# Kernel tuning notes

Measured on AMD Instinct MI355X. Metric: run time of the kernel, lower is better.

Reference implementation:

```python
import jax, jax.numpy as jnp
import numpy as np

DEPTH, DIM, DH, QH, KH = 8, 512, 64, 16, 8
B, T, S = 2, 16, 257
NUM_SPECIAL, TBE, CLAMP = 1, 4, 50.0
DI = int(DIM * 4 * 2 / 3)  # 1365
EPS = 1.1920929e-07  # torch.finfo(float32).eps used by torch RMSNorm


def _rms(x, w):
    return x * jax.lax.rsqrt(jnp.mean(jnp.square(x), -1, keepdims=True) + EPS) * w


def _l2norm(x):
    return x / jnp.maximum(jnp.linalg.norm(x, axis=-1, keepdims=True), 1e-12)


def _rotary(n):
    inv = 1.0 / (10000.0 ** (jnp.arange(0, DH, 2, dtype=jnp.float32) / DH))
    f = jnp.arange(n, dtype=jnp.float32)[:, None] * inv[None, :]
    return jnp.concatenate([f, f], -1)  # [n, DH]


def _apply_rot(rot, x):
    x1, x2 = jnp.split(x, 2, -1)
    half = jnp.concatenate([-x2, x1], -1)
    return x * jnp.cos(rot) + half * jnp.sin(rot)


def _attend(q, k, v, mask=None, causal=False):
    # q: [b, QH, n, d]; k, v: [b, KH, n, d]; GQA with groups = QH//KH
    b, hq, n, d = q.shape
    h = k.shape[1]
    g = hq // h
    qg = q.reshape(b, h, g, n, d)
    sim = jnp.einsum('bhgid,bhjd->bhgij', qg, k) * (d ** -0.5)
    sim = jnp.tanh(sim / CLAMP) * CLAMP  # softclamp
    neg = -jnp.finfo(sim.dtype).max
    if mask is not None:
        sim = jnp.where(mask, sim, neg)
    if causal:
        j = sim.shape[-1]
        cm = jnp.triu(jnp.ones((n, j), bool), j - n + 1)
        sim = jnp.where(cm, neg, sim)
    attn = jax.nn.softmax(sim, axis=-1)
    out = jnp.einsum('bhgij,bhjd->bhgid', attn, v)
    return out.reshape(b, hq, n, d)


def _attn_block(x, nw, wq, wk, wv, qg, kg, wo, rot, mask, causal):
    bn, n, _ = x.shape
    h = _rms(x, nw)
    q = (h @ wq).reshape(bn, n, QH, DH).transpose(0, 2, 1, 3)
    k = (h @ wk).reshape(bn, n, KH, DH).transpose(0, 2, 1, 3)
    v = (h @ wv).reshape(bn, n, KH, DH).transpose(0, 2, 1, 3)
    sc = DH ** 0.5
    q = _l2norm(q) * ((qg + 1.0) * sc)[:, None, :]
    k = _l2norm(k) * ((kg + 1.0) * sc)[:, None, :]
    if rot is not None:
        q = _apply_rot(rot, q)
        k = _apply_rot(rot, k)
    o = _attend(q, k, v, mask=mask, causal=causal)
    o = o.transpose(0, 2, 1, 3).reshape(bn, n, QH * DH)
    return o @ wo


def _ff(x, nw, win, bin_, wout, bout):
    h = _rms(x, nw)
    a, g = jnp.split(h @ win + bin_, 2, -1)
    return (a * jax.nn.gelu(g, approximate=False)) @ wout + bout


def setup_inputs() -> dict:
    key = jax.random.key(0)
    ks = jax.random.split(key, 8)
    s = 0.02
    return {
        'tokens': jax.random.normal(ks[0], (B, T, S, DIM), jnp.float32),
        'attn_norm_w': jnp.ones((DEPTH, DIM), jnp.float32),
        'Wq': jax.random.normal(ks[1], (DEPTH, DIM, QH * DH), jnp.float32) * s,
        'Wk': jax.random.normal(ks[2], (DEPTH, DIM, KH * DH), jnp.float32) * s,
        'Wv': jax.random.normal(ks[3], (DEPTH, DIM, KH * DH), jnp.float32) * s,
        'q_gamma': jnp.zeros((DEPTH, QH, DH), jnp.float32),
        'k_gamma': jnp.zeros((DEPTH, KH, DH), jnp.float32),
        'Wo': jax.random.normal(ks[4], (DEPTH, QH * DH, DIM), jnp.float32) * s,
        'ff_norm_w': jnp.ones((DEPTH, DIM), jnp.float32),
        'W_in': jax.random.normal(ks[5], (DEPTH, DIM, 2 * DI), jnp.float32) * s,
        'b_in': jnp.zeros((DEPTH, 2 * DI), jnp.float32),
        'W_out': jax.random.normal(ks[6], (DEPTH, DI, DIM), jnp.float32) * s,
        'b_out': jnp.zeros((DEPTH, DIM), jnp.float32),
        'final_w': jnp.ones((DIM,), jnp.float32),
    }


def reference(tokens, attn_norm_w, Wq, Wk, Wv, q_gamma, k_gamma, Wo,
              ff_norm_w, W_in, b_in, W_out, b_out, final_w):
    x = tokens  # [B, T, S, D]
    # spatial special-token mask: normal tokens cannot attend to special (rightmost) tokens
    idx = jnp.arange(S)
    is_sp = idx >= (S - NUM_SPECIAL)
    sp_mask = ~((~is_sp[:, None]) & is_sp[None, :])  # [S, S]
    sp_mask = sp_mask[None, None, None]  # broadcast over (b, h, g)
    rot = _rotary(T)
    for l in range(DEPTH):
        is_time = (l + 1) % TBE == 0
        if is_time:
            y = x.transpose(0, 2, 1, 3).reshape(B * S, T, DIM)
            o = _attn_block(y, attn_norm_w[l], Wq[l], Wk[l], Wv[l], q_gamma[l],
                            k_gamma[l], Wo[l], rot=rot, mask=None, causal=True)
            x = x + o.reshape(B, S, T, DIM).transpose(0, 2, 1, 3)
        else:
            y = x.reshape(B * T, S, DIM)
            o = _attn_block(y, attn_norm_w[l], Wq[l], Wk[l], Wv[l], q_gamma[l],
                            k_gamma[l], Wo[l], rot=None, mask=sp_mask, causal=False)
            x = x + o.reshape(B, T, S, DIM)
        x = x + _ff(x, ff_norm_w[l], W_in[l], b_in[l], W_out[l], b_out[l])
    return _rms(x, final_w)
```

## Files before the change

### kernel.cpp

```cpp
#include <hip/hip_runtime.h>
#include <hip/hip_bf16.h>
#include <math.h>

typedef __attribute__((ext_vector_type(8))) short short8;
typedef __attribute__((ext_vector_type(4))) float f32x4;
typedef __hip_bfloat16 bf16;

#define BB 2
#define TT 16
#define SSQ 257
#define DIMD 512
#define NROWS 8224
#define DII 1365
#define DI2 2730
#define FNPAD 2816
#define GLULD 1408
#define SKP 288
#define EPSR 1.1920929e-07f

__device__ __forceinline__ void async16(const void* g, const void* l) {
    __builtin_amdgcn_global_load_lds(
        (const __attribute__((address_space(1))) void*)g,
        (__attribute__((address_space(3))) void*)l, 16, 0, 0);
}

__device__ __forceinline__ short f2bfs(float x) {
    bf16 h = __float2bfloat16(x);
    return *reinterpret_cast<short*>(&h);
}

__global__ void wtrans_layer(const float* __restrict__ wq, const float* __restrict__ wk,
                             const float* __restrict__ wv, const float* __restrict__ wo,
                             const float* __restrict__ win, const float* __restrict__ wout,
                             bf16* __restrict__ dqkv, bf16* __restrict__ dwo,
                             bf16* __restrict__ dwin, bf16* __restrict__ dwout) {
    __shared__ float tile[32][33];
    int bid = blockIdx.x;
    const float* src; bf16* dst; int K, M, Kpad, interleave = 0, local;
    if (bid < 512)       { src = wq;   dst = dqkv;            K = 512;  M = 1024; Kpad = 512;  local = bid; }
    else if (bid < 768)  { src = wk;   dst = dqkv + 1024*512; K = 512;  M = 512;  Kpad = 512;  local = bid - 512; }
    else if (bid < 1024) { src = wv;   dst = dqkv + 1536*512; K = 512;  M = 512;  Kpad = 512;  local = bid - 768; }
    else if (bid < 1536) { src = wo;   dst = dwo;             K = 1024; M = 512;  Kpad = 1024; local = bid - 1024; }
    else if (bid < 2944) { src = win;  dst = dwin;            K = 512;  M = 2730; Kpad = 512;  local = bid - 1536; interleave = 1; }
    else                 { src = wout; dst = dwout;           K = 1365; M = 512;  Kpad = 1408; local = bid - 2944; }
    int tilesx = Kpad >> 5;
    int k0 = (local % tilesx) * 32, m0 = (local / tilesx) * 32;
    int tx = threadIdx.x & 31, ty = threadIdx.x >> 5;
    #pragma unroll
    for (int i = 0; i < 4; ++i) {
        int k = k0 + ty + 8 * i, m = m0 + tx;
        tile[ty + 8 * i][tx] = (k < K && m < M) ? src[(size_t)k * M + m] : 0.f;
    }
    __syncthreads();
    #pragma unroll
    for (int i = 0; i < 4; ++i) {
        int n = m0 + ty + 8 * i, k = k0 + tx;
        int nd = n;
        if (interleave) nd = (n < DII) ? 2 * n : ((n < DI2) ? 2 * (n - DII) + 1 : n);
        dst[(size_t)nd * Kpad + k] = __float2bfloat16(tile[tx][ty + 8 * i]);
    }
}

template<int BF16OUT>
__global__ __launch_bounds__(256)
void rms_kernel(const float* __restrict__ x, const float* __restrict__ w,
                void* __restrict__ out, int perm) {
    int wave = threadIdx.x >> 6, lane = threadIdx.x & 63;
    int r = blockIdx.x * 4 + wave;
    int src = r;
    if (perm) {
        int t = r & 15; int rs = r >> 4; int s = rs % SSQ; int b = rs / SSQ;
        src = (b * TT + t) * SSQ + s;
    }
    const float4* xr = (const float4*)(x + (size_t)src * DIMD) + lane * 2;
    float4 a = xr[0], c = xr[1];
    float ss = a.x*a.x + a.y*a.y + a.z*a.z + a.w*a.w
             + c.x*c.x + c.y*c.y + c.z*c.z + c.w*c.w;
    ss += __shfl_xor(ss, 1);  ss += __shfl_xor(ss, 2);  ss += __shfl_xor(ss, 4);
    ss += __shfl_xor(ss, 8);  ss += __shfl_xor(ss, 16); ss += __shfl_xor(ss, 32);
    float sc = rsqrtf(ss * (1.f / DIMD) + EPSR);
    const float4* wr = (const float4*)w + lane * 2;
    float4 wa = wr[0], wb = wr[1];
    if (BF16OUT) {
        short8 v;
        v[0] = f2bfs(a.x * sc * wa.x); v[1] = f2bfs(a.y * sc * wa.y);
        v[2] = f2bfs(a.z * sc * wa.z); v[3] = f2bfs(a.w * sc * wa.w);
        v[4] = f2bfs(c.x * sc * wb.x); v[5] = f2bfs(c.y * sc * wb.y);
        v[6] = f2bfs(c.z * sc * wb.z); v[7] = f2bfs(c.w * sc * wb.w);
        *(short8*)((bf16*)out + (size_t)r * DIMD + lane * 8) = v;
    } else {
        float4* o = (float4*)((float*)out + (size_t)r * DIMD) + lane * 2;
        float4 o0 = {a.x * sc * wa.x, a.y * sc * wa.y, a.z * sc * wa.z, a.w * sc * wa.w};
        float4 o1 = {c.x * sc * wb.x, c.y * sc * wb.y, c.z * sc * wb.z, c.w * sc * wb.w};
        o[0] = o0; o[1] = o1;
    }
}

template<int EPI, int PERM, int TM>
__global__ __launch_bounds__(256)
void mfma_gemm(const bf16* __restrict__ A, int lda,
               const bf16* __restrict__ Bt, int ldb,
               const float* __restrict__ bias,
               void* __restrict__ C, int ldc, int Mstore,
               int nrow, int K,
               const float* __restrict__ qg, const float* __restrict__ kg, int rotary) {
    constexpr int MI = TM / 32;
    constexpr int LPS = (TM == 128) ? 4 : 3;
    __shared__ __align__(16) short lds_a[3][TM * 32];
    __shared__ __align__(16) short lds_b[3][128 * 32];
    int tid = threadIdx.x;
    int wave = tid >> 6, lane = tid & 63;
    int quad = lane >> 4, l16 = lane & 15;
    int m0 = blockIdx.y * TM, n0 = blockIdx.x * 128;
    int wm = (wave & 1) * (TM / 2), wn = (wave >> 1) * 64;
    f32x4 zero4 = {0.f, 0.f, 0.f, 0.f};
    f32x4 acc[MI][4];
    #pragma unroll
    for (int i = 0; i < MI; ++i)
        #pragma unroll
        for (int j = 0; j < 4; ++j) acc[i][j] = zero4;

    const short* Ap = (const short*)A;
    const short* Bp = (const short*)Bt;
    auto aptr = [&](int g) {
        int m = g >> 2, kc = (g & 3) ^ ((g >> 3) & 3);
        int r = m0 + m; if (r >= nrow) r = nrow - 1;
        return Ap + (size_t)r * lda + kc * 8;
    };
    auto bptr = [&](int g) {
        int m = g >> 2, kc = (g & 3) ^ ((g >> 3) & 3);
        return Bp + (size_t)(n0 + m) * ldb + kc * 8;
    };
    const short* gA0; const short* gA1 = nullptr;
    int aoff0, aoff1 = 0;
    if (TM == 128) {
        gA0 = aptr(wave * 128 + lane);        aoff0 = (wave * 128) * 8;
        gA1 = aptr(wave * 128 + 64 + lane);   aoff1 = (wave * 128 + 64) * 8;
    } else {
        gA0 = aptr(wave * 64 + lane);         aoff0 = (wave * 64) * 8;
    }
    const short* gB0 = bptr(wave * 128 + lane);
    const short* gB1 = bptr(wave * 128 + 64 + lane);
    int boff0 = (wave * 128) * 8, boff1 = (wave * 128 + 64) * 8;

    auto stage = [&](int buf, int kt) {
        int ko = kt * 32;
        async16(gA0 + ko, &lds_a[buf][aoff0]);
        if (TM == 128) async16(gA1 + ko, &lds_a[buf][aoff1]);
        async16(gB0 + ko, &lds_b[buf][boff0]);
        async16(gB1 + ko, &lds_b[buf][boff1]);
    };

    int nk = K >> 5;
    stage(0, 0);
    stage(1, 1);
    int buf = 0;
    for (int kt = 0; kt < nk; ++kt) {
        if (kt + 1 < nk) {
            if constexpr (LPS == 4) asm volatile("s_waitcnt vmcnt(4)" ::: "memory");
            else                    asm volatile("s_waitcnt vmcnt(3)" ::: "memory");
        } else {
            asm volatile("s_waitcnt vmcnt(0)" ::: "memory");
        }
        __builtin_amdgcn_s_barrier();
        __builtin_amdgcn_sched_barrier(0);
        if (kt + 2 < nk) {
            int nb = buf + 2; if (nb >= 3) nb -= 3;
            stage(nb, kt + 2);
        }
        short8 af[MI], bfr[4];
        #pragma unroll
        for (int mi = 0; mi < MI; ++mi) {
            int m = wm + mi * 16 + l16;
            af[mi] = *(const short8*)&lds_a[buf][(m * 4 + (quad ^ ((m >> 1) & 3))) * 8];
        }
        #pragma unroll
        for (int nj = 0; nj < 4; ++nj) {
            int n = wn + nj * 16 + l16;
            bfr[nj] = *(const short8*)&lds_b[buf][(n * 4 + (quad ^ ((n >> 1) & 3))) * 8];
        }
        #pragma unroll
        for (int mi = 0; mi < MI; ++mi)
            #pragma unroll
            for (int nj = 0; nj < 4; ++nj)
                acc[mi][nj] = __builtin_amdgcn_mfma_f32_16x16x32_bf16(
                    af[mi], bfr[nj], acc[mi][nj], 0, 0, 0);
        ++buf; if (buf >= 3) buf = 0;
    }

    if constexpr (EPI == 1) {
        int head = (n0 + wn) >> 6;
        float gl0 = 0.f, gl1 = 0.f, gl2 = 0.f, gl3 = 0.f, inv0 = 0.f, inv1 = 0.f;
        if (head < 24) {
            const float* g = head < 16 ? qg + head * 64 : kg + (head - 16) * 64;
            gl0 = (g[l16] + 1.f) * 8.f;
            gl1 = (g[16 + l16] + 1.f) * 8.f;
            gl2 = (g[32 + l16] + 1.f) * 8.f;
            gl3 = (g[48 + l16] + 1.f) * 8.f;
            if (rotary) {
                inv0 = __expf(-(float)l16 * 0.28782313662425572f);
                inv1 = __expf(-(float)(l16 + 16) * 0.28782313662425572f);
            }
        }
        #pragma unroll
        for (int mi = 0; mi < MI; ++mi) {
            #pragma unroll
            for (int e = 0; e < 4; ++e) {
                int row = m0 + wm + mi * 16 + quad * 4 + e;
                float v0 = acc[mi][0][e], v1 = acc[mi][1][e];
                float v2 = acc[mi][2][e], v3 = acc[mi][3][e];
                if (head < 24) {
                    float ss = v0 * v0 + v1 * v1 + v2 * v2 + v3 * v3;
                    ss += __shfl_xor(ss, 1); ss += __shfl_xor(ss, 2);
                    ss += __shfl_xor(ss, 4); ss += __shfl_xor(ss, 8);
                    float invn = 1.f / fmaxf(sqrtf(ss), 1e-12f);
                    v0 *= invn * gl0; v1 *= invn * gl1;
                    v2 *= invn * gl2; v3 *= invn * gl3;
                    if (rotary) {
                        float t = (float)(row & 15);
                        float a0 = t * inv0, a1 = t * inv1;
                        float c0 = __cosf(a0), s0 = __sinf(a0);
                        float c1 = __cosf(a1), s1 = __sinf(a1);
                        float n0v = v0 * c0 - v2 * s0;
                        float n1v = v1 * c1 - v3 * s1;
                        float n2v = v2 * c0 + v0 * s0;
                        float n3v = v3 * c1 + v1 * s1;
                        v0 = n0v; v1 = n1v; v2 = n2v; v3 = n3v;
                    }
                }
                if (row < nrow) {
                    bf16* p = (bf16*)C + (size_t)row * ldc + n0 + wn + l16;
                    p[0]  = __float2bfloat16(v0);
                    p[16] = __float2bfloat16(v1);
                    p[32] = __float2bfloat16(v2);
                    p[48] = __float2bfloat16(v3);
                }
            }
        }
    } else if constexpr (EPI == 2) {
        #pragma unroll
        for (int mi = 0; mi < MI; ++mi) {
            #pragma unroll
            for (int e = 0; e < 4; ++e) {
                int row = m0 + wm + mi * 16 + quad * 4 + e;
                #pragma unroll
                for (int nj = 0; nj < 4; ++nj) {
                    int col = n0 + wn + nj * 16 + l16;
                    int j = col >> 1;
                    float b = (j < DII) ? ((col & 1) ? bias[DII + j] : bias[j]) : 0.f;
                    float v = acc[mi][nj][e] + b;
                    float prt = __shfl_xor(v, 1);
                    if (!(l16 & 1) && row < nrow) {
                        float gv = prt;
                        float glu = v * 0.5f * gv * (1.f + erff(gv * 0.70710678118654752f));
                        ((bf16*)C)[(size_t)row * ldc + j] = __float2bfloat16(glu);
                    }
                }
            }
        }
    } else {
        #pragma unroll
        for (int mi = 0; mi < MI; ++mi) {
            #pragma unroll
            for (int e = 0; e < 4; ++e) {
                int row = m0 + wm + mi * 16 + quad * 4 + e;
                if (row >= nrow) continue;
                int orow = row;
                if (PERM) {
                    int t = row & 15; int rs = row >> 4; int s = rs % SSQ; int b = rs / SSQ;
                    orow = (b * TT + t) * SSQ + s;
                }
                #pragma unroll
                for (int nj = 0; nj < 4; ++nj) {
                    int col = n0 + wn + nj * 16 + l16;
                    if (col >= Mstore) continue;
                    float v = acc[mi][nj][e];
                    if (bias) v += bias[col];
                    ((float*)C)[(size_t)orow * ldc + col] += v;
                }
            }
        }
    }
}

__global__ void vtrans_kernel(const bf16* __restrict__ qkv, bf16* __restrict__ vt) {
    int bkh = blockIdx.x;
    int kc = blockIdx.y;
    int bt = bkh >> 3, kh = bkh & 7;
    int tid = threadIdx.x;
    #pragma unroll
    for (int i = 0; i < 8; ++i) {
        int idx = tid + 256 * i;
        int kl = idx >> 6;
        int d = idx & 63;
        int key = kc * 32 + kl;
        float v = 0.f;
        if (key < SSQ)
            v = __bfloat162float(qkv[((size_t)(bt * SSQ + key)) * 2048 + 1536 + kh * 64 + d]);
        vt[((size_t)bkh * 64 + d) * SKP + key] = __float2bfloat16(v);
    }
}

__global__ __launch_bounds__(256)
void space_attn_kernel(const bf16* __restrict__ qkv, const bf16* __restrict__ vt,
                       bf16* __restrict__ ob) {
    __shared__ __align__(16) short kls[272 * 8 * 8];
    int qt = blockIdx.x, qh = blockIdx.y, bt = blockIdx.z;
    int kh = qh >> 1;
    int tid = threadIdx.x, wave = tid >> 6, lane = tid & 63;
    int quad = lane >> 4, l16 = lane & 15;
    int q0w = qt * 64 + wave * 16;
    int q = q0w + l16;
    int qc = q > 256 ? 256 : q;
    const short* qbase = (const short*)qkv + (size_t)bt * SSQ * 2048;

    const short* kgbase = qbase + 1024 + kh * 64;
    #pragma unroll
    for (int it = 0; it < 9; ++it) {
        int u = it * 4 + wave;
        if (u < 34) {
            int g = u * 64 + lane;
            int key = g >> 3, ch = g & 7;
            int srck = key < SSQ ? key : 256;
            async16(kgbase + (size_t)srck * 2048 + (ch ^ (key & 7)) * 8,
                    &kls[u * 512]);
        }
    }

    const short* qp = qbase + (size_t)qc * 2048 + qh * 64;
    short8 bq0 = *(const short8*)(qp + quad * 8);
    short8 bq1 = *(const short8*)(qp + 32 + quad * 8);
    __syncthreads();

    f32x4 zero4 = {0.f, 0.f, 0.f, 0.f};
    f32x4 sc[18];
    float sum = 0.f;
    int c0 = quad ^ (l16 & 7);
    #pragma unroll
    for (int kt = 0; kt < 17; ++kt) {
        int key = kt * 16 + l16;
        short8 ak0 = *(const short8*)&kls[(key * 8 + c0) * 8];
        short8 ak1 = *(const short8*)&kls[(key * 8 + (c0 ^ 4)) * 8];
        f32x4 cc = zero4;
        cc = __builtin_amdgcn_mfma_f32_16x16x32_bf16(ak0, bq0, cc, 0, 0, 0);
        cc = __builtin_amdgcn_mfma_f32_16x16x32_bf16(ak1, bq1, cc, 0, 0, 0);
        #pragma unroll
        for (int e = 0; e < 4; ++e) {
            float x = cc[e] * 0.0025f;
            float x2 = x * x;
            float v = cc[e] * 0.125f * (1.f + x2 * (-0.3333333333f + x2 * 0.1333333333f));
            float p = __expf(v);
            if (kt == 16) {
                bool valid = (e == 0) && (quad == 0) && (q == 256);
                p = valid ? p : 0.f;
            }
            cc[e] = p;
            sum += p;
        }
        sc[kt] = cc;
    }
    #pragma unroll
    for (int e = 0; e < 4; ++e) sc[17][e] = 0.f;
    sum += __shfl_xor(sum, 16);
    sum += __shfl_xor(sum, 32);
    float inv = __builtin_amdgcn_rcpf(sum);
    f32x4 inv4;
    #pragma unroll
    for (int e = 0; e < 4; ++e) inv4[e] = __shfl(inv, quad * 4 + e);

    f32x4 oacc[4];
    #pragma unroll
    for (int nt = 0; nt < 4; ++nt) oacc[nt] = zero4;
    const short* vbp = (const short*)vt + ((size_t)(bt * 8 + kh) * 64 + l16) * SKP;
    #pragma unroll
    for (int c8 = 0; c8 < 9; ++c8) {
        short8 pb;
        #pragma unroll
        for (int j = 0; j < 8; ++j) {
            int src_lane = ((quad & 1) * 2 + (j >> 2)) * 16 + l16;
            float v0 = __shfl(sc[2 * c8][j & 3], src_lane);
            float v1 = __shfl(sc[2 * c8 + 1][j & 3], src_lane);
            pb[j] = f2bfs(quad < 2 ? v0 : v1);
        }
        #pragma unroll
        for (int nt = 0; nt < 4; ++nt) {
            short8 av = *(const short8*)(vbp + (size_t)(nt * 16) * SKP + c8 * 32 + quad * 8);
            oacc[nt] = __builtin_amdgcn_mfma_f32_16x16x32_bf16(pb, av, oacc[nt], 0, 0, 0);
        }
    }

    #pragma unroll
    for (int e = 0; e < 4; ++e) {
        int qq = q0w + quad * 4 + e;
        if (qq <= 256) {
            bf16* op = ob + ((size_t)(bt * SSQ + qq)) * 1024 + qh * 64 + l16;
            float s = inv4[e];
            op[0]  = __float2bfloat16(oacc[0][e] * s);
            op[16] = __float2bfloat16(oacc[1][e] * s);
            op[32] = __float2bfloat16(oacc[2][e] * s);
            op[48] = __float2bfloat16(oacc[3][e] * s);
        }
    }
}

__global__ void time_attn_kernel(const bf16* __restrict__ qkv, bf16* __restrict__ ob) {
    __shared__ float qs[16][65], ks[16][65], ps[16][17];
    int bs = blockIdx.x, qh = blockIdx.y, kh = qh >> 1;
    int tid = threadIdx.x;
    size_t rowbase = (size_t)bs * 16;
    #pragma unroll
    for (int i = 0; i < 4; ++i) {
        int idx = tid + 256 * i;
        int r = idx >> 6, d = idx & 63;
        qs[r][d] = __bfloat162float(qkv[(rowbase + r) * 2048 + qh * 64 + d]);
        ks[r][d] = __bfloat162float(qkv[(rowbase + r) * 2048 + 1024 + kh * 64 + d]);
    }
    __syncthreads();
    int i = tid >> 4, j = tid & 15;
    float dot = 0.f;
    #pragma unroll 16
    for (int d = 0; d < 64; ++d) dot += qs[i][d] * ks[j][d];
    float s = dot * 0.125f;
    float x = s * 0.02f;
    float x2 = x * x;
    float v = s * (1.f + x2 * (-0.3333333333f + x2 * 0.1333333333f));
    float p = (j > i) ? 0.f : __expf(v);
    float sum = p;
    sum += __shfl_xor(sum, 1);
    sum += __shfl_xor(sum, 2);
    sum += __shfl_xor(sum, 4);
    sum += __shfl_xor(sum, 8);
    ps[i][j] = p * __builtin_amdgcn_rcpf(sum);
    __syncthreads();
    #pragma unroll
    for (int ii = 0; ii < 4; ++ii) {
        int idx = tid + 256 * ii;
        int r = idx >> 6, d = idx & 63;
        float acc = 0.f;
        #pragma unroll
        for (int jj = 0; jj < 16; ++jj)
            acc += ps[r][jj] * __bfloat162float(qkv[(rowbase + jj) * 2048 + 1536 + kh * 64 + d]);
        ob[(rowbase + r) * 1024 + qh * 64 + d] = __float2bfloat16(acc);
    }
}

extern "C" void kernel_launch(void* const* d_in, const int* in_sizes, int n_in,
                              void* d_out, int out_size, void* d_ws, size_t ws_size,
                              hipStream_t stream) {
    const float* tokens      = (const float*)d_in[0];
    const float* attn_norm_w = (const float*)d_in[1];
    const float* Wq          = (const float*)d_in[2];
    const float* Wk          = (const float*)d_in[3];
    const float* Wv          = (const float*)d_in[4];
    const float* q_gamma     = (const float*)d_in[5];
    const float* k_gamma     = (const float*)d_in[6];
    const float* Wo          = (const float*)d_in[7];
    const float* ff_norm_w   = (const float*)d_in[8];
    const float* W_in        = (const float*)d_in[9];
    const float* b_in        = (const float*)d_in[10];
    const float* W_out       = (const float*)d_in[11];
    const float* b_out       = (const float*)d_in[12];
    const float* final_w     = (const float*)d_in[13];

    float* x = (float*)d_out;
    char* ws = (char*)d_ws;

    bf16* wtqkv = (bf16*)ws;
    bf16* wto   = wtqkv + 2048 * 512;
    bf16* wtin  = wto   + 512 * 1024;
    bf16* wtout = wtin  + 2816 * 512;
    size_t off = (size_t)(2048*512 + 512*1024 + 2816*512 + 512*1408) * 2;
    bf16* h = (bf16*)(ws + off);
    off += (size_t)NROWS * 512 * 2;
    char* region = ws + off;
    bf16* qkv = (bf16*)region;
    bf16* glu = (bf16*)region;
    bf16* vt  = (bf16*)(region + (size_t)NROWS * 2048 * 2);
    bf16* ob  = (bf16*)(region + (size_t)NROWS * 2048 * 2 + (size_t)256*64*SKP*2);

    hipMemcpyAsync(x, tokens, (size_t)NROWS * 512 * 4, hipMemcpyDeviceToDevice, stream);

    for (int l = 0; l < 8; ++l) {
        int is_time = ((l + 1) % 4 == 0) ? 1 : 0;
        wtrans_layer<<<3648, 256, 0, stream>>>(
            Wq + (size_t)l * 512 * 1024, Wk + (size_t)l * 512 * 512,
            Wv + (size_t)l * 512 * 512, Wo + (size_t)l * 1024 * 512,
            W_in + (size_t)l * 512 * DI2, W_out + (size_t)l * DII * 512,
            wtqkv, wto, wtin, wtout);

        rms_kernel<1><<<2056, 256, 0, stream>>>(x, attn_norm_w + (size_t)l * 512, h, is_time);
        mfma_gemm<1, 0, 128><<<dim3(16, 65), 256, 0, stream>>>(
            h, 512, wtqkv, 512, nullptr, qkv, 2048, 2048, NROWS, 512,
            q_gamma + (size_t)l * 1024, k_gamma + (size_t)l * 512, is_time);
        if (is_time) {
            time_attn_kernel<<<dim3(514, 16), 256, 0, stream>>>(qkv, ob);
            mfma_gemm<3, 1, 64><<<dim3(4, 129), 256, 0, stream>>>(
                ob, 1024, wto, 1024, nullptr, x, 512, 512, NROWS, 1024, nullptr, nullptr, 0);
        } else {
            vtrans_kernel<<<dim3(256, 9), 256, 0, stream>>>(qkv, vt);
            space_attn_kernel<<<dim3(5, 16, 32), 256, 0, stream>>>(qkv, vt, ob);
            mfma_gemm<3, 0, 64><<<dim3(4, 129), 256, 0, stream>>>(
                ob, 1024, wto, 1024, nullptr, x, 512, 512, NROWS, 1024, nullptr, nullptr, 0);
        }

        rms_kernel<1><<<2056, 256, 0, stream>>>(x, ff_norm_w + (size_t)l * 512, h, 0);
        mfma_gemm<2, 0, 128><<<dim3(22, 65), 256, 0, stream>>>(
            h, 512, wtin, 512, b_in + (size_t)l * DI2, glu, GLULD, FNPAD, NROWS, 512,
            nullptr, nullptr, 0);
        mfma_gemm<3, 0, 64><<<dim3(4, 129), 256, 0, stream>>>(
            glu, GLULD, wtout, GLULD, b_out + (size_t)l * 512, x, 512, 512, NROWS, GLULD,
            nullptr, nullptr, 0);
    }

    rms_kernel<0><<<2056, 256, 0, stream>>>(x, final_w, x, 0);
}
```

Before: 2.308 ms.

## Enlarge GEMM M-tile, double-buffer LDS, block-interleave GLU weights, fast erf epilogue

The QKV and FF-in GEMMs now use 256-row tiles instead of 128, halving the grid rows and raising per-block reuse. The K-loop drops from a 3-buffer pipeline with manual vmcnt waits to a simpler 2-buffer scheme with __syncthreads. W_in columns are interleaved in 16-wide blocks so each lane holds the value and gate in registers, removing the shuffle. erff is replaced by an Abramowitz-Stegun polynomial approximation. This cuts epilogue and B-operand traffic, but at the cost of higher register and LDS pressure, a shallower prefetch pipeline and slight accuracy loss in GELU.

```diff
diff --git a/kernel.cpp b/kernel.cpp
--- a/kernel.cpp
+++ b/kernel.cpp
@@ -27,6 +27,17 @@
 __device__ __forceinline__ short f2bfs(float x) {
     bf16 h = __float2bfloat16(x);
     return *reinterpret_cast<short*>(&h);
+}
+
+__device__ __forceinline__ float glu_fast(float a, float g) {
+    float x = g * 0.70710678118654752f;
+    float ax = fabsf(x);
+    float t = __builtin_amdgcn_rcpf(__builtin_fmaf(0.3275911f, ax, 1.f));
+    float p = t * (0.254829592f + t * (-0.284496736f + t * (1.421413741f
+              + t * (-1.453152027f + t * 1.061405429f))));
+    float erfv = 1.f - p * __expf(-ax * ax);
+    erfv = (x < 0.f) ? -erfv : erfv;
+    return a * 0.5f * g * (1.f + erfv);
 }
 
 __global__ void wtrans_layer(const float* __restrict__ wq, const float* __restrict__ wk,
@@ -56,7 +67,12 @@
     for (int i = 0; i < 4; ++i) {
         int n = m0 + ty + 8 * i, k = k0 + tx;
         int nd = n;
-        if (interleave) nd = (n < DII) ? 2 * n : ((n < DI2) ? 2 * (n - DII) + 1 : n);
+        if (interleave) {
+            if (n < DII)        nd = ((n >> 4) << 5) + (n & 15);
+            else if (n < DI2) { int m = n - DII; nd = ((m >> 4) << 5) + 16 + (m & 15); }
+            else              { int q = n - DI2; int j = DII + (q >> 1);
+                                nd = ((j >> 4) << 5) + ((q & 1) << 4) + (j & 15); }
+        }
         dst[(size_t)nd * Kpad + k] = __float2bfloat16(tile[tx][ty + 8 * i]);
     }
 }
@@ -105,9 +121,9 @@
                int nrow, int K,
                const float* __restrict__ qg, const float* __restrict__ kg, int rotary) {
     constexpr int MI = TM / 32;
-    constexpr int LPS = (TM == 128) ? 4 : 3;
-    __shared__ __align__(16) short lds_a[3][TM * 32];
-    __shared__ __align__(16) short lds_b[3][128 * 32];
+    constexpr int ALW = TM / 64;
+    __shared__ __align__(16) short lds_a[2][TM * 32];
+    __shared__ __align__(16) short lds_b[2][128 * 32];
     int tid = threadIdx.x;
     int wave = tid >> 6, lane = tid & 63;
     int quad = lane >> 4, l16 = lane & 15;
@@ -131,13 +147,11 @@
         int m = g >> 2, kc = (g & 3) ^ ((g >> 3) & 3);
         return Bp + (size_t)(n0 + m) * ldb + kc * 8;
     };
-    const short* gA0; const short* gA1 = nullptr;
-    int aoff0, aoff1 = 0;
-    if (TM == 128) {
-        gA0 = aptr(wave * 128 + lane);        aoff0 = (wave * 128) * 8;
-        gA1 = aptr(wave * 128 + 64 + lane);   aoff1 = (wave * 128 + 64) * 8;
-    } else {
-        gA0 = aptr(wave * 64 + lane);         aoff0 = (wave * 64) * 8;
+    const short* gA[ALW]; int aoff[ALW];
+    #pragma unroll
+    for (int j = 0; j < ALW; ++j) {
+        gA[j] = aptr(wave * TM + j * 64 + lane);
+        aoff[j] = (wave * TM + j * 64) * 8;
     }
     const short* gB0 = bptr(wave * 128 + lane);
     const short* gB1 = bptr(wave * 128 + 64 + lane);
@@ -145,29 +159,19 @@
 
     auto stage = [&](int buf, int kt) {
         int ko = kt * 32;
-        async16(gA0 + ko, &lds_a[buf][aoff0]);
-        if (TM == 128) async16(gA1 + ko, &lds_a[buf][aoff1]);
+        #pragma unroll
+        for (int j = 0; j < ALW; ++j)
+            async16(gA[j] + ko, &lds_a[buf][aoff[j]]);
         async16(gB0 + ko, &lds_b[buf][boff0]);
         async16(gB1 + ko, &lds_b[buf][boff1]);
     };
 
     int nk = K >> 5;
     stage(0, 0);
-    stage(1, 1);
-    int buf = 0;
     for (int kt = 0; kt < nk; ++kt) {
-        if (kt + 1 < nk) {
-            if constexpr (LPS == 4) asm volatile("s_waitcnt vmcnt(4)" ::: "memory");
-            else                    asm volatile("s_waitcnt vmcnt(3)" ::: "memory");
-        } else {
-            asm volatile("s_waitcnt vmcnt(0)" ::: "memory");
-        }
-        __builtin_amdgcn_s_barrier();
-        __builtin_amdgcn_sched_barrier(0);
-        if (kt + 2 < nk) {
-            int nb = buf + 2; if (nb >= 3) nb -= 3;
-            stage(nb, kt + 2);
-        }
+        int buf = kt & 1;
+        __syncthreads();
+        if (kt + 1 < nk) stage(buf ^ 1, kt + 1);
         short8 af[MI], bfr[4];
         #pragma unroll
         for (int mi = 0; mi < MI; ++mi) {
@@ -185,7 +189,6 @@
             for (int nj = 0; nj < 4; ++nj)
                 acc[mi][nj] = __builtin_amdgcn_mfma_f32_16x16x32_bf16(
                     af[mi], bfr[nj], acc[mi][nj], 0, 0, 0);
-        ++buf; if (buf >= 3) buf = 0;
     }
 
     if constexpr (EPI == 1) {
@@ -238,23 +241,23 @@
             }
         }
     } else if constexpr (EPI == 2) {
+        int jbase = (n0 + wn) >> 1;
+        int j0 = jbase + l16, j1 = jbase + 16 + l16;
+        float ba0 = (j0 < DII) ? bias[j0] : 0.f;
+        float bg0 = (j0 < DII) ? bias[DII + j0] : 0.f;
+        float ba1 = (j1 < DII) ? bias[j1] : 0.f;
+        float bg1 = (j1 < DII) ? bias[DII + j1] : 0.f;
         #pragma unroll
         for (int mi = 0; mi < MI; ++mi) {
             #pragma unroll
             for (int e = 0; e < 4; ++e) {
                 int row = m0 + wm + mi * 16 + quad * 4 + e;
-                #pragma unroll
-                for (int nj = 0; nj < 4; ++nj) {
-                    int col = n0 + wn + nj * 16 + l16;
-                    int j = col >> 1;
-                    float b = (j < DII) ? ((col & 1) ? bias[DII + j] : bias[j]) : 0.f;
-                    float v = acc[mi][nj][e] + b;
-                    float prt = __shfl_xor(v, 1);
-                    if (!(l16 & 1) && row < nrow) {
-                        float gv = prt;
-                        float glu = v * 0.5f * gv * (1.f + erff(gv * 0.70710678118654752f));
-                        ((bf16*)C)[(size_t)row * ldc + j] = __float2bfloat16(glu);
-                    }
+                if (row < nrow) {
+                    bf16* cr = (bf16*)C + (size_t)row * ldc;
+                    cr[j0] = __float2bfloat16(
+                        glu_fast(acc[mi][0][e] + ba0, acc[mi][1][e] + bg0));
+                    cr[j1] = __float2bfloat16(
+                        glu_fast(acc[mi][2][e] + ba1, acc[mi][3][e] + bg1));
                 }
             }
         }
@@ -489,7 +492,7 @@
             wtqkv, wto, wtin, wtout);
 
         rms_kernel<1><<<2056, 256, 0, stream>>>(x, attn_norm_w + (size_t)l * 512, h, is_time);
-        mfma_gemm<1, 0, 128><<<dim3(16, 65), 256, 0, stream>>>(
+        mfma_gemm<1, 0, 256><<<dim3(16, 33), 256, 0, stream>>>(
             h, 512, wtqkv, 512, nullptr, qkv, 2048, 2048, NROWS, 512,
             q_gamma + (size_t)l * 1024, k_gamma + (size_t)l * 512, is_time);
         if (is_time) {
@@ -504,7 +507,7 @@
         }
 
         rms_kernel<1><<<2056, 256, 0, stream>>>(x, ff_norm_w + (size_t)l * 512, h, 0);
-        mfma_gemm<2, 0, 128><<<dim3(22, 65), 256, 0, stream>>>(
+        mfma_gemm<2, 0, 256><<<dim3(22, 33), 256, 0, stream>>>(
             h, 512, wtin, 512, b_in + (size_t)l * DI2, glu, GLULD, FNPAD, NROWS, 512,
             nullptr, nullptr, 0);
         mfma_gemm<3, 0, 64><<<dim3(4, 129), 256, 0, stream>>>(
```

After: 2.694 ms. 1.17x slower.
